# Performance work log

Hardware: AMD Instinct MI355X
Metric: run time of the kernel (lower is better)

The kernel has to match this reference:

```python
import jax, jax.numpy as jnp
import numpy as np

N_NODES = 100000
N_HEDGES = 200000
N_INC = 1000000
N_GRAPHS = 256
H = 64        # h_dim
HE = 35       # hedge_fea_dim
HOUT = 128    # hout_dim
NL = 3        # n_layers
EPS = 1e-5


def _segment_mean(vals, idx, num_segments):
    s = jax.ops.segment_sum(vals, idx, num_segments=num_segments)
    cnt = jax.ops.segment_sum(jnp.ones((vals.shape[0],), vals.dtype), idx,
                              num_segments=num_segments)
    return s / jnp.maximum(cnt, 1.0)[:, None]


def _bn(z, g, b):
    # training-mode BatchNorm1d: batch stats, biased variance
    m = jnp.mean(z, axis=0)
    v = jnp.var(z, axis=0)
    return (z - m) * jax.lax.rsqrt(v + EPS) * g + b


def setup_inputs() -> dict:
    key = jax.random.key(0)
    ks = jax.random.split(key, 32)
    inp = {
        "x": jax.random.normal(ks[0], (N_NODES, 92), jnp.float32),
        "node_idx": jax.random.randint(ks[1], (N_INC,), 0, N_NODES),
        "hedge_idx": jax.random.randint(ks[2], (N_INC,), 0, N_HEDGES),
        "hedge_attr": jax.random.normal(ks[3], (N_HEDGES, HE), jnp.float32),
        "batch": jnp.sort(jax.random.randint(ks[4], (N_NODES,), 0, N_GRAPHS)),
    }
    s = 0.05
    cat = H + HE  # 99
    inp["embed_w"] = jax.random.normal(ks[5], (92, H), jnp.float32) * s
    inp["embed_b"] = jnp.zeros((H,), jnp.float32)
    inp["f1_w"] = jax.random.normal(ks[6], (NL, cat, HE), jnp.float32) * s
    inp["f1_b"] = jnp.zeros((NL, HE), jnp.float32)
    inp["c1_w"] = jax.random.normal(ks[7], (NL, cat, HE), jnp.float32) * s
    inp["c1_b"] = jnp.zeros((NL, HE), jnp.float32)
    inp["f2_w"] = jax.random.normal(ks[8], (NL, cat, H), jnp.float32) * s
    inp["f2_b"] = jnp.zeros((NL, H), jnp.float32)
    inp["c2_w"] = jax.random.normal(ks[9], (NL, cat, H), jnp.float32) * s
    inp["c2_b"] = jnp.zeros((NL, H), jnp.float32)
    inp["bnf_g"] = jnp.ones((NL, HE), jnp.float32)
    inp["bnf_b"] = jnp.zeros((NL, HE), jnp.float32)
    inp["bnc_g"] = jnp.ones((NL, HE), jnp.float32)
    inp["bnc_b"] = jnp.zeros((NL, HE), jnp.float32)
    inp["bno_g"] = jnp.ones((NL, H), jnp.float32)
    inp["bno_b"] = jnp.zeros((NL, H), jnp.float32)
    inp["l2_w"] = jax.random.normal(ks[10], (H, HOUT), jnp.float32) * s
    inp["l2_b"] = jnp.zeros((HOUT,), jnp.float32)
    inp["out_w"] = jax.random.normal(ks[11], (HOUT, 1), jnp.float32) * s
    inp["out_b"] = jnp.zeros((1,), jnp.float32)
    return inp


def reference(x, node_idx, hedge_idx, hedge_attr, batch,
              embed_w, embed_b, f1_w, f1_b, c1_w, c1_b,
              f2_w, f2_b, c2_w, c2_b,
              bnf_g, bnf_b, bnc_g, bnc_b, bno_g, bno_b,
              l2_w, l2_b, out_w, out_b):
    sp = jax.nn.softplus
    x = x @ embed_w + embed_b  # [N, H]
    for i in range(NL):
        # gather node feats per incidence, mean over each hyperedge
        hx = _segment_mean(x[node_idx], hedge_idx, N_HEDGES)       # [NH, H]
        msg = jnp.concatenate([hx, hedge_attr], axis=1)            # [NH, H+HE]
        z_f = _bn(msg @ f1_w[i] + f1_b[i], bnf_g[i], bnf_b[i])
        z_c = _bn(msg @ c1_w[i] + c1_b[i], bnc_g[i], bnc_b[i])
        hedge_attr = jax.nn.sigmoid(z_f) * sp(z_c)                 # [NH, HE]
        z = jnp.concatenate([x[node_idx], hedge_attr[hedge_idx]], axis=-1)  # [E, H+HE]
        o = jax.nn.sigmoid(z @ f2_w[i] + f2_b[i]) * sp(z @ c2_w[i] + c2_b[i])  # [E, H]
        o = _segment_mean(o, node_idx, N_NODES)                    # [N, H]
        o = _bn(o, bno_g[i], bno_b[i])
        x = sp(o + x)
    pooled = _segment_mean(x, batch, N_GRAPHS)                     # [G, H]
    h = sp(pooled @ l2_w + l2_b)                                   # [G, HOUT]
    return h @ out_w + out_b                                       # [G, 1]
```

## Files before the change

kernel.cpp:

```cpp
#include <hip/hip_runtime.h>
#include <math.h>

#define N_NODES 100000
#define N_HEDGES 200000
#define N_INC 1000000
#define N_GRAPHS 256
#define HD 64
#define HE 35
#define CAT 99
#define EPSB 1e-5f

typedef __attribute__((ext_vector_type(8))) short short8;
typedef __attribute__((ext_vector_type(4))) float f32x4;

__device__ __forceinline__ float sp_f(float x) {
  return fmaxf(x, 0.f) + __logf(1.f + __expf(-fabsf(x)));
}
__device__ __forceinline__ float sig_f(float x) {
  return __builtin_amdgcn_rcpf(1.f + __expf(-x));
}
__device__ __forceinline__ unsigned bfr(float x) {
  unsigned u = __float_as_uint(x);
  return (u + 0x7fffu + ((u >> 16) & 1u)) >> 16;
}
__device__ __forceinline__ unsigned pk2(float lo, float hi) {
  return bfr(lo) | (bfr(hi) << 16);
}
__device__ __forceinline__ float blo(unsigned v) { return __uint_as_float(v << 16); }
__device__ __forceinline__ float bhi(unsigned v) {
  return __uint_as_float(v & 0xffff0000u);
}
__device__ __forceinline__ float bf2f(unsigned short s) {
  return __uint_as_float(((unsigned)s) << 16);
}

__global__ __launch_bounds__(256) void k_hist(const int* __restrict__ nidx,
                                              const int* __restrict__ hidx,
                                              int* __restrict__ degN,
                                              int* __restrict__ degH,
                                              int* __restrict__ rankN,
                                              int* __restrict__ rankH) {
  int e = blockIdx.x * 256 + threadIdx.x;
  if (e >= N_INC) return;
  rankH[e] = atomicAdd(&degH[hidx[e]], 1);
  rankN[e] = atomicAdd(&degN[nidx[e]], 1);
}

#define CHB ((N_HEDGES + 255) / 256)
#define CNB ((N_NODES + 255) / 256)
__global__ __launch_bounds__(256) void k_alloc2(const int* __restrict__ degH,
                                                const int* __restrict__ degN,
                                                int* __restrict__ offH,
                                                int* __restrict__ offN,
                                                int* __restrict__ gctr) {
  __shared__ int s[256];
  __shared__ int base;
  int b = blockIdx.x, t = threadIdx.x;
  const int* deg;
  int* off;
  int n, i;
  int* ctr;
  if (b < CHB) {
    deg = degH; off = offH; n = N_HEDGES; ctr = &gctr[0]; i = b * 256 + t;
  } else {
    deg = degN; off = offN; n = N_NODES; ctr = &gctr[1]; i = (b - CHB) * 256 + t;
  }
  int d = (i < n) ? deg[i] : 0;
  s[t] = d;
  __syncthreads();
  for (int st = 1; st < 256; st <<= 1) {
    int u = 0;
    if (t >= st) u = s[t - st];
    __syncthreads();
    if (t >= st) s[t] += u;
    __syncthreads();
  }
  if (t == 255) base = atomicAdd(ctr, s[255]);
  __syncthreads();
  if (i < n) off[i] = s[t] - d + base;
}

__global__ __launch_bounds__(256) void k_fill(const int* __restrict__ nidx,
                                              const int* __restrict__ hidx,
                                              const int* __restrict__ rankH,
                                              const int* __restrict__ rankN,
                                              const int* __restrict__ offH,
                                              const int* __restrict__ offN,
                                              int* __restrict__ permHn,
                                              int* __restrict__ permNh) {
  int e = blockIdx.x * 256 + threadIdx.x;
  if (e >= N_INC) return;
  int nd = nidx[e], hg = hidx[e];
  permHn[offH[hg] + rankH[e]] = nd;
  permNh[offN[nd] + rankN[e]] = hg;
}

__global__ __launch_bounds__(64) void k_wpack(const float* __restrict__ f1w,
                                              const float* __restrict__ c1w,
                                              uint4* __restrict__ wpk) {
  int b = blockIdx.x;
  int layer = b / 20, rem = b % 20, ct = rem / 4, ks = rem % 4;
  int lane = threadIdx.x;
  int col = ct * 16 + (lane & 15);
  int k0 = ks * 32 + (lane >> 4) * 8;
  const float* wf = f1w + layer * CAT * HE;
  const float* wc = c1w + layer * CAT * HE;
  unsigned v[4];
#pragma unroll
  for (int p = 0; p < 4; ++p) {
    float lo = 0.f, hi = 0.f;
    int ka = k0 + p * 2, kb = ka + 1;
    if (ka < 99) {
      if (col < 35) lo = wf[ka * 35 + col];
      else if (col >= 36 && col < 71) lo = wc[ka * 35 + (col - 36)];
    }
    if (kb < 99) {
      if (col < 35) hi = wf[kb * 35 + col];
      else if (col >= 36 && col < 71) hi = wc[kb * 35 + (col - 36)];
    }
    v[p] = pk2(lo, hi);
  }
  uint4 o;
  o.x = v[0]; o.y = v[1]; o.z = v[2]; o.w = v[3];
  wpk[b * 64 + lane] = o;
}

__global__ __launch_bounds__(256) void k_cvt_ha(const float* __restrict__ src,
                                                unsigned short* __restrict__ dst,
                                                int n) {
  int t = blockIdx.x * 256 + threadIdx.x;
  if (t < n) dst[t] = (unsigned short)bfr(src[t]);
}

__global__ __launch_bounds__(256) void k_embed(const float* __restrict__ x,
                                               const float* __restrict__ w,
                                               const float* __restrict__ b,
                                               unsigned short* __restrict__ outb) {
  __shared__ float ws[92 * 64];
  __shared__ float rs[16][93];
  int tid = threadIdx.x;
  for (int i = tid; i < 92 * 64; i += 256) ws[i] = w[i];
  int r0 = blockIdx.x * 16;
  for (int i = tid; i < 16 * 92; i += 256) {
    int r = i / 92, k = i - r * 92;
    rs[r][k] = x[(r0 + r) * 92 + k];
  }
  __syncthreads();
  int h = tid & 63;
  float bias = b[h];
  for (int rr = tid >> 6; rr < 16; rr += 4) {
    float acc = bias;
    for (int k = 0; k < 92; ++k) acc += rs[rr][k] * ws[k * 64 + h];
    outb[(r0 + rr) * 64 + h] = (unsigned short)bfr(acc);
  }
}

#define GR 128
__global__ __launch_bounds__(256) void k_hedge_gemm(
    const unsigned short* __restrict__ xb, const int* __restrict__ permHn,
    const int* __restrict__ offH, const int* __restrict__ degH,
    const unsigned short* __restrict__ hab, const uint4* __restrict__ wpk,
    float* __restrict__ z, float* __restrict__ stats) {
  __shared__ unsigned short msg[GR * 128];
  __shared__ float ps[160];
  int tid = threadIdx.x;
  int w = tid >> 6, lane = tid & 63;
  int r0 = blockIdx.x * GR;
  if (tid < 160) ps[tid] = 0.f;

  short8 bfg[5][4];
#pragma unroll
  for (int ct = 0; ct < 5; ++ct)
#pragma unroll
    for (int ks = 0; ks < 4; ++ks)
      bfg[ct][ks] = __builtin_bit_cast(short8, wpk[(ct * 4 + ks) * 64 + lane]);

  char* mb = (char*)msg;
  for (int r = 0; r < 32; ++r) {
    int rloc = w * 32 + r;
    int row = r0 + rloc;
    float acc = 0.f;
    unsigned short hv = 0;
    if (row < N_HEDGES) {
      int o = offH[row], d = degH[row];
      int k = 0;
      for (; k + 4 <= d; k += 4) {
        int n0 = permHn[o + k], n1 = permHn[o + k + 1];
        int n2 = permHn[o + k + 2], n3 = permHn[o + k + 3];
        acc += (bf2f(xb[(size_t)n0 * 64 + lane]) + bf2f(xb[(size_t)n1 * 64 + lane])) +
               (bf2f(xb[(size_t)n2 * 64 + lane]) + bf2f(xb[(size_t)n3 * 64 + lane]));
      }
      for (; k < d; ++k) acc += bf2f(xb[(size_t)permHn[o + k] * 64 + lane]);
      acc *= 1.f / (float)max(d, 1);
      if (lane < 35) hv = hab[(size_t)row * 35 + lane];
    }
    int swz = (rloc & 7) << 4;
    *(unsigned short*)(mb + ((rloc * 256 + lane * 2) ^ swz)) = (unsigned short)bfr(acc);
    *(unsigned short*)(mb + ((rloc * 256 + 128 + lane * 2) ^ swz)) = hv;
  }
  __syncthreads();

#pragma unroll
  for (int rt = 0; rt < 2; ++rt) {
    int rloc = w * 32 + rt * 16 + (lane & 15);
    short8 a[4];
#pragma unroll
    for (int ks = 0; ks < 4; ++ks) {
      int byte = rloc * 256 + (ks * 32 + (lane >> 4) * 8) * 2;
      a[ks] = *(const short8*)(mb + (byte ^ ((rloc & 7) << 4)));
    }
#pragma unroll
    for (int ct = 0; ct < 5; ++ct) {
      f32x4 acc = {0.f, 0.f, 0.f, 0.f};
#pragma unroll
      for (int ks = 0; ks < 4; ++ks)
        acc = __builtin_amdgcn_mfma_f32_16x16x32_bf16(a[ks], bfg[ct][ks], acc, 0, 0, 0);
      float s = (acc[0] + acc[1]) + (acc[2] + acc[3]);
      float q = (acc[0] * acc[0] + acc[1] * acc[1]) +
                (acc[2] * acc[2] + acc[3] * acc[3]);
      s += __shfl_xor(s, 16);
      s += __shfl_xor(s, 32);
      q += __shfl_xor(q, 16);
      q += __shfl_xor(q, 32);
      int col = ct * 16 + (lane & 15);
      if ((lane >> 4) == 0 && col < 72) {
        atomicAdd(&ps[col], s);
        atomicAdd(&ps[80 + col], q);
      }
      int growb = r0 + w * 32 + rt * 16 + ((lane >> 4) << 2);
      if (col < 72) {
#pragma unroll
        for (int r = 0; r < 4; ++r) {
          int grow = growb + r;
          if (grow < N_HEDGES) z[(size_t)grow * 72 + col] = acc[r];
        }
      }
    }
  }
  __syncthreads();
  if (tid < 160) atomicAdd(&stats[tid], ps[tid]);
}

__global__ __launch_bounds__(256) void k_hedge_apply(
    const float* __restrict__ z, const float* __restrict__ stats,
    const float* __restrict__ gf, const float* __restrict__ bf_,
    const float* __restrict__ gc, const float* __restrict__ bc_,
    unsigned short* __restrict__ hab) {
  int t = blockIdx.x * 256 + threadIdx.x;
  if (t >= N_HEDGES * 35) return;
  int r = t / 35, c = t - r * 35;
  const float inv = 1.f / N_HEDGES;
  float mf = stats[c] * inv;
  float vf = stats[80 + c] * inv - mf * mf;
  float mc = stats[36 + c] * inv;
  float vc = stats[116 + c] * inv - mc * mc;
  const float* zr = &z[(size_t)r * 72];
  float nf = (zr[c] - mf) * rsqrtf(vf + EPSB) * gf[c] + bf_[c];
  float nc = (zr[36 + c] - mc) * rsqrtf(vc + EPSB) * gc[c] + bc_[c];
  hab[t] = (unsigned short)bfr(sig_f(nf) * sp_f(nc));
}

__global__ __launch_bounds__(256) void k_uv_node(const unsigned short* __restrict__ xb,
                                                 const float* __restrict__ f2w,
                                                 const float* __restrict__ c2w,
                                                 unsigned* __restrict__ Ufc) {
  __shared__ float wf[64 * 64];
  __shared__ float wc[64 * 64];
  __shared__ float rs[16][65];
  int tid = threadIdx.x;
  for (int i = tid; i < 64 * 64; i += 256) {
    wf[i] = f2w[i];
    wc[i] = c2w[i];
  }
  int r0 = blockIdx.x * 16;
  for (int i = tid; i < 16 * 64; i += 256) {
    int r = i >> 6, k = i & 63;
    rs[r][k] = bf2f(xb[(size_t)(r0 + r) * 64 + k]);
  }
  __syncthreads();
  int h = tid & 63, rb = tid >> 6;
  float af0 = 0, af1 = 0, af2 = 0, af3 = 0, ac0 = 0, ac1 = 0, ac2 = 0, ac3 = 0;
  for (int k = 0; k < 64; ++k) {
    float wfv = wf[k * 64 + h], wcv = wc[k * 64 + h];
    float m0 = rs[rb][k], m1 = rs[rb + 4][k], m2 = rs[rb + 8][k], m3 = rs[rb + 12][k];
    af0 += m0 * wfv; ac0 += m0 * wcv;
    af1 += m1 * wfv; ac1 += m1 * wcv;
    af2 += m2 * wfv; ac2 += m2 * wcv;
    af3 += m3 * wfv; ac3 += m3 * wcv;
  }
  int row = r0 + rb;
  Ufc[row * 64 + h] = pk2(af0, ac0);
  Ufc[(row + 4) * 64 + h] = pk2(af1, ac1);
  Ufc[(row + 8) * 64 + h] = pk2(af2, ac2);
  Ufc[(row + 12) * 64 + h] = pk2(af3, ac3);
}

__global__ __launch_bounds__(256) void k_uv_hedge(
    const unsigned short* __restrict__ hab, const float* __restrict__ f2wb,
    const float* __restrict__ c2wb, const float* __restrict__ f2b,
    const float* __restrict__ c2b, unsigned* __restrict__ Vfc) {
  __shared__ float wf[35 * 64];
  __shared__ float wc[35 * 64];
  __shared__ float rs[16][36];
  int tid = threadIdx.x;
  for (int i = tid; i < 35 * 64; i += 256) {
    wf[i] = f2wb[i];
    wc[i] = c2wb[i];
  }
  int r0 = blockIdx.x * 16;
  for (int i = tid; i < 16 * 35; i += 256) {
    int r = i / 35, k = i - r * 35;
    rs[r][k] = bf2f(hab[(r0 + r) * 35 + k]);
  }
  __syncthreads();
  int h = tid & 63, rb = tid >> 6;
  float af0, af1, af2, af3, ac0, ac1, ac2, ac3;
  af0 = af1 = af2 = af3 = f2b[h];
  ac0 = ac1 = ac2 = ac3 = c2b[h];
  for (int k = 0; k < 35; ++k) {
    float wfv = wf[k * 64 + h], wcv = wc[k * 64 + h];
    float m0 = rs[rb][k], m1 = rs[rb + 4][k], m2 = rs[rb + 8][k], m3 = rs[rb + 12][k];
    af0 += m0 * wfv; ac0 += m0 * wcv;
    af1 += m1 * wfv; ac1 += m1 * wcv;
    af2 += m2 * wfv; ac2 += m2 * wcv;
    af3 += m3 * wfv; ac3 += m3 * wcv;
  }
  int row = r0 + rb;
  Vfc[row * 64 + h] = pk2(af0, ac0);
  Vfc[(row + 4) * 64 + h] = pk2(af1, ac1);
  Vfc[(row + 8) * 64 + h] = pk2(af2, ac2);
  Vfc[(row + 12) * 64 + h] = pk2(af3, ac3);
}

__device__ __forceinline__ float act2(float uf, float uc, unsigned v) {
  float a = uf + blo(v);
  float b = uc + bhi(v);
  return sig_f(a) * sp_f(b);
}
__global__ __launch_bounds__(256) void k_node_aggr(const int* __restrict__ permNh,
                                                   const int* __restrict__ offN,
                                                   const int* __restrict__ degN,
                                                   const unsigned* __restrict__ Ufc,
                                                   const unsigned* __restrict__ Vfc,
                                                   float* __restrict__ o) {
  int gt = blockIdx.x * 256 + threadIdx.x;
  int wid = gt >> 6, h = gt & 63;
  if (wid >= N_NODES) return;
  int off = offN[wid], d = degN[wid];
  unsigned u = Ufc[wid * 64 + h];
  float uf = blo(u), uc = bhi(u);
  float acc = 0.f;
  int k = 0;
  for (; k + 4 <= d; k += 4) {
    int h0 = permNh[off + k], h1 = permNh[off + k + 1];
    int h2 = permNh[off + k + 2], h3 = permNh[off + k + 3];
    unsigned v0 = Vfc[h0 * 64 + h];
    unsigned v1 = Vfc[h1 * 64 + h];
    unsigned v2 = Vfc[h2 * 64 + h];
    unsigned v3 = Vfc[h3 * 64 + h];
    acc += (act2(uf, uc, v0) + act2(uf, uc, v1)) +
           (act2(uf, uc, v2) + act2(uf, uc, v3));
  }
  for (; k < d; ++k) acc += act2(uf, uc, Vfc[permNh[off + k] * 64 + h]);
  o[wid * 64 + h] = acc / (float)max(d, 1);
}

__global__ __launch_bounds__(256) void k_ostats(const float* __restrict__ o,
                                                float* __restrict__ stats) {
  int h = threadIdx.x & 63;
  int rs = threadIdx.x >> 6;
  float s = 0.f, sq = 0.f;
  for (int r = blockIdx.x * 4 + rs; r < N_NODES; r += gridDim.x * 4) {
    float v = o[r * 64 + h];
    s += v;
    sq += v * v;
  }
  __shared__ float ls[4][2][64];
  ls[rs][0][h] = s;
  ls[rs][1][h] = sq;
  __syncthreads();
  if (threadIdx.x < 64) {
    float ts = ls[0][0][h] + ls[1][0][h] + ls[2][0][h] + ls[3][0][h];
    float tq = ls[0][1][h] + ls[1][1][h] + ls[2][1][h] + ls[3][1][h];
    atomicAdd(&stats[h], ts);
    atomicAdd(&stats[64 + h], tq);
  }
}

__global__ __launch_bounds__(256) void k_update(unsigned short* __restrict__ xb,
                                                const float* __restrict__ o,
                                                const float* __restrict__ stats,
                                                const float* __restrict__ g,
                                                const float* __restrict__ b) {
  int t = blockIdx.x * 256 + threadIdx.x;
  int h = t & 63;
  float mean = stats[h] * (1.f / N_NODES);
  float var = stats[64 + h] * (1.f / N_NODES) - mean * mean;
  float is = rsqrtf(var + EPSB);
  float v = (o[t] - mean) * is * g[h] + b[h];
  float r = sp_f(v + bf2f(xb[t]));
  xb[t] = (unsigned short)bfr(r);
}

#define PR 512
__global__ __launch_bounds__(256) void k_pool(const unsigned short* __restrict__ xb,
                                              const int* __restrict__ batch,
                                              float* __restrict__ pooled,
                                              float* __restrict__ gcnt) {
  int h = threadIdx.x & 63, rs = threadIdx.x >> 6;
  int r0 = blockIdx.x * PR;
  int rend = min(r0 + PR, N_NODES);
  int gcur = -1;
  float acc = 0.f;
  int cnt = 0;
  for (int r = r0 + rs; r < rend; r += 4) {
    int g = batch[r];
    if (g != gcur) {
      if (gcur >= 0) {
        atomicAdd(&pooled[gcur * 64 + h], acc);
        if (h == 0) atomicAdd(&gcnt[gcur], (float)cnt);
      }
      gcur = g;
      acc = 0.f;
      cnt = 0;
    }
    acc += bf2f(xb[(size_t)r * 64 + h]);
    cnt++;
  }
  if (gcur >= 0) {
    atomicAdd(&pooled[gcur * 64 + h], acc);
    if (h == 0) atomicAdd(&gcnt[gcur], (float)cnt);
  }
}

__global__ __launch_bounds__(128) void k_final(const float* __restrict__ pooled,
                                               const float* __restrict__ gcnt,
                                               const float* __restrict__ l2w,
                                               const float* __restrict__ l2b,
                                               const float* __restrict__ ow,
                                               const float* __restrict__ ob,
                                               float* __restrict__ out) {
  int g = blockIdx.x;
  int t = threadIdx.x;
  __shared__ float row[64];
  __shared__ float hh[128];
  if (t < 64) row[t] = pooled[g * 64 + t] / fmaxf(gcnt[g], 1.f);
  __syncthreads();
  float acc = l2b[t];
  for (int k = 0; k < 64; ++k) acc += row[k] * l2w[k * 128 + t];
  hh[t] = sp_f(acc) * ow[t];
  __syncthreads();
  for (int s = 64; s > 0; s >>= 1) {
    if (t < s) hh[t] += hh[t + s];
    __syncthreads();
  }
  if (t == 0) out[g] = hh[0] + ob[0];
}

extern "C" void kernel_launch(void* const* d_in, const int* in_sizes, int n_in,
                              void* d_out, int out_size, void* d_ws, size_t ws_size,
                              hipStream_t stream) {
  const float* x_in = (const float*)d_in[0];
  const int* node_idx = (const int*)d_in[1];
  const int* hedge_idx = (const int*)d_in[2];
  const float* hedge_attr = (const float*)d_in[3];
  const int* batch = (const int*)d_in[4];
  const float* embed_w = (const float*)d_in[5];
  const float* embed_b = (const float*)d_in[6];
  const float* f1_w = (const float*)d_in[7];
  const float* c1_w = (const float*)d_in[9];
  const float* f2_w = (const float*)d_in[11];
  const float* f2_b = (const float*)d_in[12];
  const float* c2_w = (const float*)d_in[13];
  const float* c2_b = (const float*)d_in[14];
  const float* bnf_g = (const float*)d_in[15];
  const float* bnf_b = (const float*)d_in[16];
  const float* bnc_g = (const float*)d_in[17];
  const float* bnc_b = (const float*)d_in[18];
  const float* bno_g = (const float*)d_in[19];
  const float* bno_b = (const float*)d_in[20];
  const float* l2_w = (const float*)d_in[21];
  const float* l2_b = (const float*)d_in[22];
  const float* out_w = (const float*)d_in[23];
  const float* out_b = (const float*)d_in[24];

  char* base = (char*)d_ws;
  size_t off = 0;
  auto alloc = [&](size_t bytes) {
    size_t o = off;
    off = (off + bytes + 255) & ~(size_t)255;
    return o;
  };
  unsigned short* xbf = (unsigned short*)(base + alloc((size_t)N_NODES * 64 * 2));
  unsigned short* hab = (unsigned short*)(base + alloc((size_t)N_HEDGES * 35 * 2));
  unsigned* Vfc = (unsigned*)(base + alloc((size_t)N_HEDGES * 64 * 4));
  float* obuf = (float*)(base + alloc((size_t)N_NODES * 64 * 4));
  float* zbuf = (float*)Vfc;
  unsigned* Ufc = (unsigned*)(base + alloc((size_t)N_NODES * 64 * 4));
  uint4* wpk = (uint4*)(base + alloc((size_t)60 * 64 * 16));
  float* hstatsA = (float*)(base + alloc(3 * 160 * 4));
  float* ostatsA = (float*)(base + alloc(3 * 128 * 4));
  float* pooled = (float*)(base + alloc((size_t)N_GRAPHS * 64 * 4));
  float* gcnt = (float*)(base + alloc((size_t)N_GRAPHS * 4));
  int* degH = (int*)(base + alloc((size_t)N_HEDGES * 4));
  int* degN = (int*)(base + alloc((size_t)N_NODES * 4));
  int* gctr = (int*)(base + alloc(2 * 4));
  int* offH = (int*)(base + alloc((size_t)N_HEDGES * 4));
  int* offN = (int*)(base + alloc((size_t)N_NODES * 4));
  int* rankH = (int*)(base + alloc((size_t)N_INC * 4));
  int* rankN = (int*)(base + alloc((size_t)N_INC * 4));
  int* permHn = (int*)(base + alloc((size_t)N_INC * 4));
  int* permNh = (int*)(base + alloc((size_t)N_INC * 4));
  (void)ws_size;
  (void)in_sizes;
  (void)n_in;
  (void)out_size;

  hipMemsetAsync(degH, 0, (size_t)((char*)gctr - (char*)degH) + 2 * 4, stream);
  k_hist<<<(N_INC + 255) / 256, 256, 0, stream>>>(node_idx, hedge_idx, degN, degH,
                                                  rankN, rankH);
  k_alloc2<<<CHB + CNB, 256, 0, stream>>>(degH, degN, offH, offN, gctr);
  k_fill<<<(N_INC + 255) / 256, 256, 0, stream>>>(node_idx, hedge_idx, rankH, rankN,
                                                  offH, offN, permHn, permNh);
  k_wpack<<<60, 64, 0, stream>>>(f1_w, c1_w, wpk);
  k_cvt_ha<<<(N_HEDGES * 35 + 255) / 256, 256, 0, stream>>>(hedge_attr, hab,
                                                            N_HEDGES * 35);
  k_embed<<<N_NODES / 16, 256, 0, stream>>>(x_in, embed_w, embed_b, xbf);

  hipMemsetAsync(hstatsA, 0, (size_t)((char*)ostatsA - (char*)hstatsA) + 3 * 128 * 4,
                 stream);

  for (int i = 0; i < 3; ++i) {
    float* hstats = hstatsA + i * 160;
    float* ostats = ostatsA + i * 128;

    k_hedge_gemm<<<(N_HEDGES + GR - 1) / GR, 256, 0, stream>>>(
        xbf, permHn, offH, degH, hab, wpk + (size_t)i * 20 * 64, zbuf, hstats);
    k_hedge_apply<<<(N_HEDGES * 35 + 255) / 256, 256, 0, stream>>>(
        zbuf, hstats, bnf_g + i * HE, bnf_b + i * HE, bnc_g + i * HE, bnc_b + i * HE,
        hab);

    k_uv_node<<<N_NODES / 16, 256, 0, stream>>>(xbf, f2_w + i * CAT * 64,
                                                c2_w + i * CAT * 64, Ufc);
    k_uv_hedge<<<N_HEDGES / 16, 256, 0, stream>>>(
        hab, f2_w + i * CAT * 64 + 64 * 64, c2_w + i * CAT * 64 + 64 * 64,
        f2_b + i * 64, c2_b + i * 64, Vfc);

    k_node_aggr<<<N_NODES * 64 / 256, 256, 0, stream>>>(permNh, offN, degN, Ufc, Vfc,
                                                        obuf);

    k_ostats<<<1024, 256, 0, stream>>>(obuf, ostats);
    k_update<<<N_NODES * 64 / 256, 256, 0, stream>>>(xbf, obuf, ostats,
                                                     bno_g + i * 64, bno_b + i * 64);
  }

  hipMemsetAsync(pooled, 0, (size_t)((char*)gcnt - (char*)pooled) + N_GRAPHS * 4,
                 stream);
  k_pool<<<(N_NODES + PR - 1) / PR, 256, 0, stream>>>(xbf, batch, pooled, gcnt);
  k_final<<<N_GRAPHS, 128, 0, stream>>>(pooled, gcnt, l2_w, l2_b, out_w, out_b,
                                        (float*)d_out);
}
```

Before: 1.386 ms.

## Aggregate hyperedge features edge-parallel into LDS with ordered CSR offsets

The one-atomic-per-block offset allocation is replaced by a block-sum plus scan, so hyperedge CSR offsets come out in hyperedge order. A block of 128 hyperedges therefore owns one contiguous incidence range. The hedge GEMM now walks that range flat: it loads (node, hedge) pairs and 16-byte node-feature vectors and accumulates them into an LDS fp32 buffer with shared-memory atomics. This replaces the per-row serial gather loop that was sensitive to degree skew. Inverse degrees are precomputed, and the z intermediate is stored as bf16 to halve its traffic, which trades some precision for the batch-norm inputs.

```diff
diff --git a/kernel.cpp b/kernel.cpp
--- a/kernel.cpp
+++ b/kernel.cpp
@@ -48,22 +48,63 @@
 
 #define CHB ((N_HEDGES + 255) / 256)
 #define CNB ((N_NODES + 255) / 256)
+
+__global__ __launch_bounds__(256) void k_bsum(const int* __restrict__ degH,
+                                              const int* __restrict__ degN,
+                                              int* __restrict__ bsum) {
+  __shared__ int s[256];
+  int b = blockIdx.x, t = threadIdx.x;
+  const int* deg;
+  int n, i;
+  if (b < CHB) {
+    deg = degH; n = N_HEDGES; i = b * 256 + t;
+  } else {
+    deg = degN; n = N_NODES; i = (b - CHB) * 256 + t;
+  }
+  s[t] = (i < n) ? deg[i] : 0;
+  __syncthreads();
+  for (int st = 128; st > 0; st >>= 1) {
+    if (t < st) s[t] += s[t + st];
+    __syncthreads();
+  }
+  if (t == 0) bsum[b] = s[0];
+}
+
+__global__ __launch_bounds__(64) void k_bscan(int* __restrict__ bsum) {
+  int seg0 = (blockIdx.x == 0) ? 0 : CHB;
+  int segn = (blockIdx.x == 0) ? CHB : CNB;
+  int lane = threadIdx.x;
+  int carry = 0;
+  for (int base = 0; base < segn; base += 64) {
+    int i = base + lane;
+    int orig = (i < segn) ? bsum[seg0 + i] : 0;
+    int v = orig;
+    for (int st = 1; st < 64; st <<= 1) {
+      int u = __shfl_up(v, st);
+      if (lane >= st) v += u;
+    }
+    int total = __shfl(v, 63);
+    if (i < segn) bsum[seg0 + i] = carry + (v - orig);
+    carry += total;
+  }
+}
+
 __global__ __launch_bounds__(256) void k_alloc2(const int* __restrict__ degH,
                                                 const int* __restrict__ degN,
+                                                const int* __restrict__ bsum,
                                                 int* __restrict__ offH,
                                                 int* __restrict__ offN,
-                                                int* __restrict__ gctr) {
+                                                float* __restrict__ invdH) {
   __shared__ int s[256];
-  __shared__ int base;
   int b = blockIdx.x, t = threadIdx.x;
   const int* deg;
   int* off;
   int n, i;
-  int* ctr;
-  if (b < CHB) {
-    deg = degH; off = offH; n = N_HEDGES; ctr = &gctr[0]; i = b * 256 + t;
+  bool isH = (b < CHB);
+  if (isH) {
+    deg = degH; off = offH; n = N_HEDGES; i = b * 256 + t;
   } else {
-    deg = degN; off = offN; n = N_NODES; ctr = &gctr[1]; i = (b - CHB) * 256 + t;
+    deg = degN; off = offN; n = N_NODES; i = (b - CHB) * 256 + t;
   }
   int d = (i < n) ? deg[i] : 0;
   s[t] = d;
@@ -75,9 +116,10 @@
     if (t >= st) s[t] += u;
     __syncthreads();
   }
-  if (t == 255) base = atomicAdd(ctr, s[255]);
-  __syncthreads();
-  if (i < n) off[i] = s[t] - d + base;
+  if (i < n) {
+    off[i] = s[t] - d + bsum[b];
+    if (isH) invdH[i] = 1.f / (float)max(d, 1);
+  }
 }
 
 __global__ __launch_bounds__(256) void k_fill(const int* __restrict__ nidx,
@@ -86,12 +128,12 @@
                                               const int* __restrict__ rankN,
                                               const int* __restrict__ offH,
                                               const int* __restrict__ offN,
-                                              int* __restrict__ permHn,
+                                              int2* __restrict__ pairH,
                                               int* __restrict__ permNh) {
   int e = blockIdx.x * 256 + threadIdx.x;
   if (e >= N_INC) return;
   int nd = nidx[e], hg = hidx[e];
-  permHn[offH[hg] + rankH[e]] = nd;
+  pairH[offH[hg] + rankH[e]] = make_int2(nd, hg);
   permNh[offN[nd] + rankN[e]] = hg;
 }
 
@@ -157,16 +199,15 @@
 
 #define GR 128
 __global__ __launch_bounds__(256) void k_hedge_gemm(
-    const unsigned short* __restrict__ xb, const int* __restrict__ permHn,
-    const int* __restrict__ offH, const int* __restrict__ degH,
+    const unsigned short* __restrict__ xb, const int2* __restrict__ pairH,
+    const int* __restrict__ offH, const float* __restrict__ invdH,
     const unsigned short* __restrict__ hab, const uint4* __restrict__ wpk,
-    float* __restrict__ z, float* __restrict__ stats) {
-  __shared__ unsigned short msg[GR * 128];
+    unsigned short* __restrict__ z, float* __restrict__ stats) {
+  __shared__ float facc[GR * 64];
   __shared__ float ps[160];
   int tid = threadIdx.x;
   int w = tid >> 6, lane = tid & 63;
   int r0 = blockIdx.x * GR;
-  if (tid < 160) ps[tid] = 0.f;
 
   short8 bfg[5][4];
 #pragma unroll
@@ -175,30 +216,43 @@
     for (int ks = 0; ks < 4; ++ks)
       bfg[ct][ks] = __builtin_bit_cast(short8, wpk[(ct * 4 + ks) * 64 + lane]);
 
-  char* mb = (char*)msg;
+  for (int i = tid; i < GR * 64; i += 256) facc[i] = 0.f;
+  if (tid < 160) ps[tid] = 0.f;
+  int p0 = offH[r0];
+  int p1 = (r0 + GR < N_HEDGES) ? offH[r0 + GR] : N_INC;
+  __syncthreads();
+
+  int n8 = (p1 - p0) * 8;
+  for (int i = tid; i < n8; i += 256) {
+    int entry = i >> 3, c8 = i & 7;
+    int2 pr = pairH[p0 + entry];
+    int fb = (pr.y - r0) * 64 + c8 * 8;
+    uint4 xv = *(const uint4*)(xb + (size_t)pr.x * 64 + c8 * 8);
+    atomicAdd(&facc[fb + 0], blo(xv.x));
+    atomicAdd(&facc[fb + 1], bhi(xv.x));
+    atomicAdd(&facc[fb + 2], blo(xv.y));
+    atomicAdd(&facc[fb + 3], bhi(xv.y));
+    atomicAdd(&facc[fb + 4], blo(xv.z));
+    atomicAdd(&facc[fb + 5], bhi(xv.z));
+    atomicAdd(&facc[fb + 6], blo(xv.w));
+    atomicAdd(&facc[fb + 7], bhi(xv.w));
+  }
+  __syncthreads();
+
+  char* mb = (char*)facc;
   for (int r = 0; r < 32; ++r) {
     int rloc = w * 32 + r;
     int row = r0 + rloc;
-    float acc = 0.f;
-    unsigned short hv = 0;
+    float v = facc[rloc * 64 + lane];
+    unsigned short mv = 0, hv = 0;
     if (row < N_HEDGES) {
-      int o = offH[row], d = degH[row];
-      int k = 0;
-      for (; k + 4 <= d; k += 4) {
-        int n0 = permHn[o + k], n1 = permHn[o + k + 1];
-        int n2 = permHn[o + k + 2], n3 = permHn[o + k + 3];
-        acc += (bf2f(xb[(size_t)n0 * 64 + lane]) + bf2f(xb[(size_t)n1 * 64 + lane])) +
-               (bf2f(xb[(size_t)n2 * 64 + lane]) + bf2f(xb[(size_t)n3 * 64 + lane]));
-      }
-      for (; k < d; ++k) acc += bf2f(xb[(size_t)permHn[o + k] * 64 + lane]);
-      acc *= 1.f / (float)max(d, 1);
+      mv = (unsigned short)bfr(v * invdH[row]);
       if (lane < 35) hv = hab[(size_t)row * 35 + lane];
     }
     int swz = (rloc & 7) << 4;
-    *(unsigned short*)(mb + ((rloc * 256 + lane * 2) ^ swz)) = (unsigned short)bfr(acc);
+    *(unsigned short*)(mb + ((rloc * 256 + lane * 2) ^ swz)) = mv;
     *(unsigned short*)(mb + ((rloc * 256 + 128 + lane * 2) ^ swz)) = hv;
   }
-  __syncthreads();
 
 #pragma unroll
   for (int rt = 0; rt < 2; ++rt) {
@@ -232,7 +286,8 @@
 #pragma unroll
         for (int r = 0; r < 4; ++r) {
           int grow = growb + r;
-          if (grow < N_HEDGES) z[(size_t)grow * 72 + col] = acc[r];
+          if (grow < N_HEDGES)
+            z[(size_t)grow * 72 + col] = (unsigned short)bfr(acc[r]);
         }
       }
     }
@@ -242,7 +297,7 @@
 }
 
 __global__ __launch_bounds__(256) void k_hedge_apply(
-    const float* __restrict__ z, const float* __restrict__ stats,
+    const unsigned short* __restrict__ z, const float* __restrict__ stats,
     const float* __restrict__ gf, const float* __restrict__ bf_,
     const float* __restrict__ gc, const float* __restrict__ bc_,
     unsigned short* __restrict__ hab) {
@@ -254,9 +309,9 @@
   float vf = stats[80 + c] * inv - mf * mf;
   float mc = stats[36 + c] * inv;
   float vc = stats[116 + c] * inv - mc * mc;
-  const float* zr = &z[(size_t)r * 72];
-  float nf = (zr[c] - mf) * rsqrtf(vf + EPSB) * gf[c] + bf_[c];
-  float nc = (zr[36 + c] - mc) * rsqrtf(vc + EPSB) * gc[c] + bc_[c];
+  const unsigned short* zr = &z[(size_t)r * 72];
+  float nf = (bf2f(zr[c]) - mf) * rsqrtf(vf + EPSB) * gf[c] + bf_[c];
+  float nc = (bf2f(zr[36 + c]) - mc) * rsqrtf(vc + EPSB) * gc[c] + bc_[c];
   hab[t] = (unsigned short)bfr(sig_f(nf) * sp_f(nc));
 }
 
@@ -495,7 +550,7 @@
   unsigned short* hab = (unsigned short*)(base + alloc((size_t)N_HEDGES * 35 * 2));
   unsigned* Vfc = (unsigned*)(base + alloc((size_t)N_HEDGES * 64 * 4));
   float* obuf = (float*)(base + alloc((size_t)N_NODES * 64 * 4));
-  float* zbuf = (float*)Vfc;
+  unsigned short* zbuf = (unsigned short*)Vfc;
   unsigned* Ufc = (unsigned*)(base + alloc((size_t)N_NODES * 64 * 4));
   uint4* wpk = (uint4*)(base + alloc((size_t)60 * 64 * 16));
   float* hstatsA = (float*)(base + alloc(3 * 160 * 4));
@@ -504,24 +559,28 @@
   float* gcnt = (float*)(base + alloc((size_t)N_GRAPHS * 4));
   int* degH = (int*)(base + alloc((size_t)N_HEDGES * 4));
   int* degN = (int*)(base + alloc((size_t)N_NODES * 4));
-  int* gctr = (int*)(base + alloc(2 * 4));
   int* offH = (int*)(base + alloc((size_t)N_HEDGES * 4));
   int* offN = (int*)(base + alloc((size_t)N_NODES * 4));
+  float* invdH = (float*)(base + alloc((size_t)N_HEDGES * 4));
+  int* bsum = (int*)(base + alloc((size_t)(CHB + CNB) * 4));
   int* rankH = (int*)(base + alloc((size_t)N_INC * 4));
   int* rankN = (int*)(base + alloc((size_t)N_INC * 4));
-  int* permHn = (int*)(base + alloc((size_t)N_INC * 4));
+  int2* pairH = (int2*)(base + alloc((size_t)N_INC * 8));
   int* permNh = (int*)(base + alloc((size_t)N_INC * 4));
   (void)ws_size;
   (void)in_sizes;
   (void)n_in;
   (void)out_size;
 
-  hipMemsetAsync(degH, 0, (size_t)((char*)gctr - (char*)degH) + 2 * 4, stream);
+  hipMemsetAsync(degH, 0,
+                 (size_t)((char*)degN - (char*)degH) + (size_t)N_NODES * 4, stream);
   k_hist<<<(N_INC + 255) / 256, 256, 0, stream>>>(node_idx, hedge_idx, degN, degH,
                                                   rankN, rankH);
-  k_alloc2<<<CHB + CNB, 256, 0, stream>>>(degH, degN, offH, offN, gctr);
+  k_bsum<<<CHB + CNB, 256, 0, stream>>>(degH, degN, bsum);
+  k_bscan<<<2, 64, 0, stream>>>(bsum);
+  k_alloc2<<<CHB + CNB, 256, 0, stream>>>(degH, degN, bsum, offH, offN, invdH);
   k_fill<<<(N_INC + 255) / 256, 256, 0, stream>>>(node_idx, hedge_idx, rankH, rankN,
-                                                  offH, offN, permHn, permNh);
+                                                  offH, offN, pairH, permNh);
   k_wpack<<<60, 64, 0, stream>>>(f1_w, c1_w, wpk);
   k_cvt_ha<<<(N_HEDGES * 35 + 255) / 256, 256, 0, stream>>>(hedge_attr, hab,
                                                             N_HEDGES * 35);
@@ -535,7 +594,7 @@
     float* ostats = ostatsA + i * 128;
 
     k_hedge_gemm<<<(N_HEDGES + GR - 1) / GR, 256, 0, stream>>>(
-        xbf, permHn, offH, degH, hab, wpk + (size_t)i * 20 * 64, zbuf, hstats);
+        xbf, pairH, offH, invdH, hab, wpk + (size_t)i * 20 * 64, zbuf, hstats);
     k_hedge_apply<<<(N_HEDGES * 35 + 255) / 256, 256, 0, stream>>>(
         zbuf, hstats, bnf_g + i * HE, bnf_b + i * HE, bnc_g + i * HE, bnc_b + i * HE,
         hab);
```

After: 2.107 ms. +52.0%, slower.
